# Performance work log

Hardware: AMD Instinct MI355X
Metric: run time of the kernel (lower is better)

The kernel has to match this reference:

```python
import jax, jax.numpy as jnp
import numpy as np

NUM_POINTS = 7
SCALES = (0.25, 0.125, 0.0625, 0.03125)
LENS_AREA = (8, 25)
OUTPUT_SIZES = ((8, 32), (8, 64))
CANON_SCALE = 224.0  # LevelMapper defaults (ctor's 160 is not forwarded)
CANON_LVL = 4.0
K_MIN, K_MAX = 2.0, 5.0
EPS = 1e-6


def _boundary_interp(pts, wp):
    # pts: [N, n, 2] polyline; sample wp points uniformly in arc parameter
    n = pts.shape[1]
    u = (jnp.arange(wp, dtype=pts.dtype) + 0.5) / wp * (n - 1)
    i0 = jnp.clip(jnp.floor(u).astype(jnp.int32), 0, n - 2)
    f = (u - i0.astype(pts.dtype))[None, :, None]
    return pts[:, i0] * (1 - f) + pts[:, i0 + 1] * f  # [N, wp, 2]


def _make_grid(polys_norm, hp, wp):
    # polys_norm: [N, 2n, 2] normalized to [0,1]; first n = top l->r, last n = bottom l->r
    n = polys_norm.shape[1] // 2
    top = _boundary_interp(polys_norm[:, :n], wp)
    bot = _boundary_interp(polys_norm[:, n:], wp)
    v = ((jnp.arange(hp, dtype=polys_norm.dtype) + 0.5) / hp)[None, :, None, None]
    return top[:, None] * (1 - v) + bot[:, None] * v  # [N, hp, wp, 2] (x,y)


def _bilinear(feat, img_ids, grid):
    # feat [B,C,H,W]; grid normalized [0,1] image coords -> pixel coords of this level
    B, C, H, W = feat.shape
    x = grid[..., 0] * W - 0.5
    y = grid[..., 1] * H - 0.5
    x0 = jnp.floor(x)
    y0 = jnp.floor(y)
    wx = (x - x0)[..., None]
    wy = (y - y0)[..., None]
    x0i = x0.astype(jnp.int32)
    y0i = y0.astype(jnp.int32)
    ids = img_ids[:, None, None]

    def g(xi, yi):
        xc = jnp.clip(xi, 0, W - 1)
        yc = jnp.clip(yi, 0, H - 1)
        val = feat[ids, :, yc, xc]  # [N, hp, wp, C]
        m = ((xi >= 0) & (xi < W) & (yi >= 0) & (yi < H))[..., None]
        return val * m.astype(feat.dtype)

    out = (g(x0i, y0i) * (1 - wx) * (1 - wy)
           + g(x0i + 1, y0i) * wx * (1 - wy)
           + g(x0i, y0i + 1) * (1 - wx) * wy
           + g(x0i + 1, y0i + 1) * wx * wy)
    return jnp.transpose(out, (0, 3, 1, 2))  # [N, C, hp, wp]


def _forward(feats, polys, img_ids, lens):
    n = NUM_POINTS
    idx = list(range(n)) + list(range(n, 2 * n))[::-1]  # top l->r, bottom flipped l->r
    H0, W0 = feats[0].shape[-2:]
    wh = jnp.array([W0 / SCALES[0], H0 / SCALES[0]], dtype=feats[0].dtype)
    polys_norm = polys[:, idx] / wh
    # FPN level routing from bbox area of the polygon (boxlist.area heuristic)
    s = jnp.sqrt((polys[..., 0].max(1) - polys[..., 0].min(1))
                 * (polys[..., 1].max(1) - polys[..., 1].min(1)))
    lvl = jnp.clip(jnp.floor(CANON_LVL + jnp.log2(s / CANON_SCALE + EPS)),
                   K_MIN, K_MAX).astype(jnp.int32) - int(K_MIN)
    # text-length bucket -> pooler id (first bucket whose len_max >= len)
    thr = jnp.array(LENS_AREA[:-1], dtype=lens.dtype)
    pooler_id = jnp.sum(lens[:, None] > thr[None, :], axis=1).astype(jnp.int32)

    outs = []
    N, C = polys.shape[0], feats[0].shape[1]
    for pid, (hp, wp) in enumerate(OUTPUT_SIZES):
        grid = _make_grid(polys_norm, hp, wp)
        acc = jnp.zeros((N, C, hp, wp), feats[0].dtype)
        for l, f in enumerate(feats):
            sel = ((lvl == l) & (pooler_id == pid))[:, None, None, None]
            acc = jnp.where(sel, _bilinear(f, img_ids, grid), acc)
        outs.append(acc)
    return tuple(outs)


def setup_inputs() -> dict:
    B, C, H0, W0 = 2, 256, 200, 336
    N, n = 256, NUM_POINTS
    key = jax.random.key(0)
    k0, k1, k2, k3 = jax.random.split(key, 4)
    feat0 = jax.random.normal(k0, (B, C, H0, W0), jnp.float32)
    feat1 = jax.random.normal(k1, (B, C, H0 // 2, W0 // 2), jnp.float32)
    feat2 = jax.random.normal(k2, (B, C, H0 // 4, W0 // 4), jnp.float32)
    feat3 = jax.random.normal(k3, (B, C, H0 // 8, W0 // 8), jnp.float32)
    rng = np.random.default_rng(0)
    img_w, img_h = W0 / SCALES[0], H0 / SCALES[0]
    cx = rng.uniform(0.25, 0.75, N) * img_w
    cy = rng.uniform(0.2, 0.8, N) * img_h
    w = rng.uniform(40.0, 600.0, N)
    h = rng.uniform(16.0, 80.0, N)
    t = np.linspace(0.0, 1.0, n)
    top_x = cx[:, None] + (t[None, :] - 0.5) * w[:, None]
    top_y = cy[:, None] - h[:, None] / 2 + rng.uniform(-2, 2, (N, n))
    bot_y = cy[:, None] + h[:, None] / 2 + rng.uniform(-2, 2, (N, n))
    # stored polygon order: top l->r then bottom r->l (matches self.idx reorder)
    top = np.stack([top_x, top_y], -1)
    bot = np.stack([top_x[:, ::-1], bot_y[:, ::-1]], -1)
    polys = jnp.asarray(np.concatenate([top, bot], 1), jnp.float32)  # [N, 14, 2]
    img_ids = jnp.asarray(rng.integers(0, B, N), jnp.int32)
    lens = jnp.asarray(rng.integers(1, 25, N), jnp.int32)
    return {"feat0": feat0, "feat1": feat1, "feat2": feat2, "feat3": feat3,
            "polys": polys, "img_ids": img_ids, "lens": lens}


def reference(feat0, feat1, feat2, feat3, polys, img_ids, lens):
    return _forward((feat0, feat1, feat2, feat3), polys, img_ids, lens)
```

## Files before the change

### kernel.cpp

```cpp
#include <hip/hip_runtime.h>


#define NBOX 256
#define NCH  256
#define HP   8
#define CCHUNK 32
#define OUT0_ELEMS ((size_t)NBOX * NCH * HP * 32)

typedef float f32x4 __attribute__((ext_vector_type(4)));

__device__ __forceinline__ void make_geo(
    const float* __restrict__ pts, int pos, int lwp, int W, int H,
    int& o00, int& o10, int& o01, int& o11,
    float& w00, float& w10, float& w01, float& w11)
{
    const int wp = 1 << lwp;
    const int i  = pos >> lwp;
    const int j  = pos & (wp - 1);

    float u  = ((j + 0.5f) / (float)wp) * 6.0f;
    int   i0 = (int)floorf(u);
    i0 = min(max(i0, 0), 5);
    float f = u - (float)i0;

    float txa = pts[2 * i0]     / 1344.0f, tya = pts[2 * i0 + 1] / 800.0f;
    float txb = pts[2 * i0 + 2] / 1344.0f, tyb = pts[2 * i0 + 3] / 800.0f;
    int ka = 13 - i0, kb = 12 - i0;
    float bxa = pts[2 * ka] / 1344.0f, bya = pts[2 * ka + 1] / 800.0f;
    float bxb = pts[2 * kb] / 1344.0f, byb = pts[2 * kb + 1] / 800.0f;

    float topx = txa * (1.0f - f) + txb * f;
    float topy = tya * (1.0f - f) + tyb * f;
    float botx = bxa * (1.0f - f) + bxb * f;
    float boty = bya * (1.0f - f) + byb * f;

    float v  = (i + 0.5f) / 8.0f;
    float gx = topx * (1.0f - v) + botx * v;
    float gy = topy * (1.0f - v) + boty * v;

    float x = gx * (float)W - 0.5f;
    float y = gy * (float)H - 0.5f;
    float x0f = floorf(x), y0f = floorf(y);
    float fx = x - x0f,   fy = y - y0f;
    int x0 = (int)x0f, y0 = (int)y0f;
    int x1 = x0 + 1,   y1 = y0 + 1;

    int x0c = min(max(x0, 0), W - 1), x1c = min(max(x1, 0), W - 1);
    int y0c = min(max(y0, 0), H - 1), y1c = min(max(y1, 0), H - 1);
    float m00 = (x0 >= 0 && x0 < W && y0 >= 0 && y0 < H) ? 1.0f : 0.0f;
    float m10 = (x1 >= 0 && x1 < W && y0 >= 0 && y0 < H) ? 1.0f : 0.0f;
    float m01 = (x0 >= 0 && x0 < W && y1 >= 0 && y1 < H) ? 1.0f : 0.0f;
    float m11 = (x1 >= 0 && x1 < W && y1 >= 0 && y1 < H) ? 1.0f : 0.0f;

    o00 = y0c * W + x0c;  o10 = y0c * W + x1c;
    o01 = y1c * W + x0c;  o11 = y1c * W + x1c;
    w00 = (1.0f - fx) * (1.0f - fy) * m00;
    w10 = fx * (1.0f - fy) * m10;
    w01 = (1.0f - fx) * fy * m01;
    w11 = fx * fy * m11;
}

__global__ __launch_bounds__(256) void poly_pool_kernel(
    const float* __restrict__ f0, const float* __restrict__ f1,
    const float* __restrict__ f2, const float* __restrict__ f3,
    const float* __restrict__ polys, const int* __restrict__ img_ids,
    const int* __restrict__ lens, float* __restrict__ out)
{
    const int b    = blockIdx.y;
    const int pidk = blockIdx.z;
    const int lwp  = 5 + pidk;
    const int npos = HP << lwp;
    const int c0   = blockIdx.x * CCHUNK;
    const int tid  = threadIdx.x;

    float* outb = out + (pidk ? OUT0_ELEMS : (size_t)0) + (size_t)b * NCH * npos;

    const int pooler = (lens[b] > 8) ? 1 : 0;
    if (pooler != pidk) {
        f32x4 z = (f32x4)(0.0f);
        f32x4* p = reinterpret_cast<f32x4*>(outb + (size_t)c0 * npos);
        const int total4 = (CCHUNK * npos) >> 2;
        for (int k = tid; k < total4; k += 256)
            __builtin_nontemporal_store(z, p + k);
        return;
    }

    __shared__ float pts[28];
    if (tid < 28) pts[tid] = polys[b * 28 + tid];
    __syncthreads();

    float minx = pts[0], maxx = pts[0], miny = pts[1], maxy = pts[1];
#pragma unroll
    for (int k = 1; k < 14; ++k) {
        float x = pts[2 * k], y = pts[2 * k + 1];
        minx = fminf(minx, x); maxx = fmaxf(maxx, x);
        miny = fminf(miny, y); maxy = fmaxf(maxy, y);
    }
    float s = sqrtf((maxx - minx) * (maxy - miny));
    int lvl = (int)floorf(4.0f + log2f(s / 224.0f + 1e-6f));
    lvl = min(max(lvl, 2), 5) - 2;

    const float* feat; int H, W;
    switch (lvl) {
        case 0:  feat = f0; H = 200; W = 336; break;
        case 1:  feat = f1; H = 100; W = 168; break;
        case 2:  feat = f2; H = 50;  W = 84;  break;
        default: feat = f3; H = 25;  W = 42;  break;
    }
    const int img = img_ids[b];
    const int HW  = H * W;
    const float* featimg = feat + (size_t)img * NCH * HW;
    const float* fbase   = featimg + (size_t)c0 * HW;

    int   o00, o10, o01, o11;
    float w00, w10, w01, w11;
    make_geo(pts, tid, lwp, W, H, o00, o10, o01, o11, w00, w10, w01, w11);

    float* op = outb + (size_t)c0 * npos + tid;

    if (!pidk) {
        for (int c = 0; c < CCHUNK; c += 8) {
            float t00[8], t10[8], t01[8], t11[8];
#pragma unroll
            for (int k = 0; k < 8; ++k) {
                const float* fc = fbase + (size_t)(c + k) * HW;
                t00[k] = fc[o00]; t10[k] = fc[o10];
                t01[k] = fc[o01]; t11[k] = fc[o11];
            }
#pragma unroll
            for (int k = 0; k < 8; ++k) {
                float r = w00 * t00[k] + w10 * t10[k] + w01 * t01[k] + w11 * t11[k];
                __builtin_nontemporal_store(r, op + (size_t)(c + k) * 256);
            }
        }
    } else {
        int   q00, q10, q01, q11;
        float v00, v10, v01, v11;
        make_geo(pts, tid + 256, lwp, W, H, q00, q10, q01, q11, v00, v10, v01, v11);

        for (int c = 0; c < CCHUNK; c += 4) {
            float t00[4], t10[4], t01[4], t11[4];
            float s00[4], s10[4], s01[4], s11[4];
#pragma unroll
            for (int k = 0; k < 4; ++k) {
                const float* fc = fbase + (size_t)(c + k) * HW;
                t00[k] = fc[o00]; t10[k] = fc[o10];
                t01[k] = fc[o01]; t11[k] = fc[o11];
                s00[k] = fc[q00]; s10[k] = fc[q10];
                s01[k] = fc[q01]; s11[k] = fc[q11];
            }
#pragma unroll
            for (int k = 0; k < 4; ++k) {
                float r0 = w00 * t00[k] + w10 * t10[k] + w01 * t01[k] + w11 * t11[k];
                float r1 = v00 * s00[k] + v10 * s10[k] + v01 * s01[k] + v11 * s11[k];
                __builtin_nontemporal_store(r0, op + (size_t)(c + k) * 512);
                __builtin_nontemporal_store(r1, op + (size_t)(c + k) * 512 + 256);
            }
        }
    }
}

extern "C" void kernel_launch(void* const* d_in, const int* in_sizes, int n_in,
                              void* d_out, int out_size, void* d_ws, size_t ws_size,
                              hipStream_t stream) {
    const float* f0    = (const float*)d_in[0];
    const float* f1    = (const float*)d_in[1];
    const float* f2    = (const float*)d_in[2];
    const float* f3    = (const float*)d_in[3];
    const float* polys = (const float*)d_in[4];
    const int*   ids   = (const int*)d_in[5];
    const int*   lens  = (const int*)d_in[6];
    float* out = (float*)d_out;

    dim3 grid(NCH / CCHUNK, NBOX, 2);
    poly_pool_kernel<<<grid, 256, 0, stream>>>(f0, f1, f2, f3, polys, ids, lens, out);
}
```

Before: 355.0 us.

## Stage polygon bounding-box feature patch in LDS before bilinear sampling

Computes the polygon's bounding box at the chosen FPN level and cooperatively loads that patch for 4 channels at a time into shared memory using coalesced row loads. The bilinear taps then read from LDS instead of doing scattered global gathers. Large patches fall back to a direct gather path. This adds 40KB of LDS per block, which lowers occupancy, plus two barriers per round and loads of patch pixels that may never be sampled.

```diff
diff --git a/kernel.cpp b/kernel.cpp
--- a/kernel.cpp
+++ b/kernel.cpp
@@ -5,13 +5,15 @@
 #define NCH  256
 #define HP   8
 #define CCHUNK 32
+#define NSTG 4
+#define PMAX 2560
 #define OUT0_ELEMS ((size_t)NBOX * NCH * HP * 32)
 
 typedef float f32x4 __attribute__((ext_vector_type(4)));
 
 __device__ __forceinline__ void make_geo(
     const float* __restrict__ pts, int pos, int lwp, int W, int H,
-    int& o00, int& o10, int& o01, int& o11,
+    int& x0c, int& x1c, int& y0c, int& y1c,
     float& w00, float& w10, float& w01, float& w11)
 {
     const int wp = 1 << lwp;
@@ -45,15 +47,13 @@
     int x0 = (int)x0f, y0 = (int)y0f;
     int x1 = x0 + 1,   y1 = y0 + 1;
 
-    int x0c = min(max(x0, 0), W - 1), x1c = min(max(x1, 0), W - 1);
-    int y0c = min(max(y0, 0), H - 1), y1c = min(max(y1, 0), H - 1);
+    x0c = min(max(x0, 0), W - 1); x1c = min(max(x1, 0), W - 1);
+    y0c = min(max(y0, 0), H - 1); y1c = min(max(y1, 0), H - 1);
     float m00 = (x0 >= 0 && x0 < W && y0 >= 0 && y0 < H) ? 1.0f : 0.0f;
     float m10 = (x1 >= 0 && x1 < W && y0 >= 0 && y0 < H) ? 1.0f : 0.0f;
     float m01 = (x0 >= 0 && x0 < W && y1 >= 0 && y1 < H) ? 1.0f : 0.0f;
     float m11 = (x1 >= 0 && x1 < W && y1 >= 0 && y1 < H) ? 1.0f : 0.0f;
 
-    o00 = y0c * W + x0c;  o10 = y0c * W + x1c;
-    o01 = y1c * W + x0c;  o11 = y1c * W + x1c;
     w00 = (1.0f - fx) * (1.0f - fy) * m00;
     w10 = fx * (1.0f - fy) * m10;
     w01 = (1.0f - fx) * fy * m01;
@@ -86,6 +86,7 @@
     }
 
     __shared__ float pts[28];
+    __shared__ float patch[NSTG][PMAX];
     if (tid < 28) pts[tid] = polys[b * 28 + tid];
     __syncthreads();
 
@@ -110,51 +111,92 @@
     const int img = img_ids[b];
     const int HW  = H * W;
     const float* featimg = feat + (size_t)img * NCH * HW;
-    const float* fbase   = featimg + (size_t)c0 * HW;
-
-    int   o00, o10, o01, o11;
+
+    float sxn = (float)W / 1344.0f, syn = (float)H / 800.0f;
+    int px0 = min(max((int)floorf(minx * sxn - 0.5f), 0), W - 1);
+    int px1 = min(max((int)floorf(maxx * sxn - 0.5f) + 1, 0), W - 1);
+    int py0 = min(max((int)floorf(miny * syn - 0.5f), 0), H - 1);
+    int py1 = min(max((int)floorf(maxy * syn - 0.5f) + 1, 0), H - 1);
+    const int PW = px1 - px0 + 1;
+    const int PH = py1 - py0 + 1;
+    const int lg = (PW <= 64) ? 6 : ((PW <= 128) ? 7 : 8);
+    const int PWP = 1 << lg;
+    const int npatch = PH << lg;
+    const bool staged = (PW <= 256) && (npatch <= PMAX);
+
+    int   x0c, x1c, y0c, y1c;
     float w00, w10, w01, w11;
-    make_geo(pts, tid, lwp, W, H, o00, o10, o01, o11, w00, w10, w01, w11);
+    make_geo(pts, tid, lwp, W, H, x0c, x1c, y0c, y1c, w00, w10, w01, w11);
+    int   x0d = 0, x1d = 0, y0d = 0, y1d = 0;
+    float v00 = 0, v10 = 0, v01 = 0, v11 = 0;
+    if (pidk)
+        make_geo(pts, tid + 256, lwp, W, H, x0d, x1d, y0d, y1d, v00, v10, v01, v11);
 
     float* op = outb + (size_t)c0 * npos + tid;
 
-    if (!pidk) {
-        for (int c = 0; c < CCHUNK; c += 8) {
-            float t00[8], t10[8], t01[8], t11[8];
+    if (staged) {
+        const int o00 = ((y0c - py0) << lg) + (x0c - px0);
+        const int o10 = ((y0c - py0) << lg) + (x1c - px0);
+        const int o01 = ((y1c - py0) << lg) + (x0c - px0);
+        const int o11 = ((y1c - py0) << lg) + (x1c - px0);
+        int q00 = 0, q10 = 0, q01 = 0, q11 = 0;
+        if (pidk) {
+            q00 = ((y0d - py0) << lg) + (x0d - px0);
+            q10 = ((y0d - py0) << lg) + (x1d - px0);
+            q01 = ((y1d - py0) << lg) + (x0d - px0);
+            q11 = ((y1d - py0) << lg) + (x1d - px0);
+        }
+
+        for (int rnd = 0; rnd < CCHUNK / NSTG; ++rnd) {
+            const float* sb = featimg + (size_t)(c0 + rnd * NSTG) * HW
+                              + (size_t)py0 * W + px0;
+            for (int e = tid; e < npatch; e += 512) {
+                int eb = min(e + 256, npatch - 1);
+                int ra = e  >> lg, ca = min(e  & (PWP - 1), PW - 1);
+                int rb = eb >> lg, cb = min(eb & (PWP - 1), PW - 1);
+                const float* sA = sb + ra * W + ca;
+                const float* sB = sb + rb * W + cb;
+                float a0 = sA[0], a1 = sA[HW], a2 = sA[2 * HW], a3 = sA[3 * HW];
+                float b0 = sB[0], b1 = sB[HW], b2 = sB[2 * HW], b3 = sB[3 * HW];
+                patch[0][e]  = a0; patch[1][e]  = a1;
+                patch[2][e]  = a2; patch[3][e]  = a3;
+                patch[0][eb] = b0; patch[1][eb] = b1;
+                patch[2][eb] = b2; patch[3][eb] = b3;
+            }
+            __syncthreads();
+
 #pragma unroll
-            for (int k = 0; k < 8; ++k) {
-                const float* fc = fbase + (size_t)(c + k) * HW;
-                t00[k] = fc[o00]; t10[k] = fc[o10];
-                t01[k] = fc[o01]; t11[k] = fc[o11];
-            }
+            for (int k = 0; k < NSTG; ++k) {
+                float r0 = w00 * patch[k][o00] + w10 * patch[k][o10]
+                         + w01 * patch[k][o01] + w11 * patch[k][o11];
+                __builtin_nontemporal_store(r0, op + (size_t)(rnd * NSTG + k) * npos);
+            }
+            if (pidk) {
 #pragma unroll
-            for (int k = 0; k < 8; ++k) {
-                float r = w00 * t00[k] + w10 * t10[k] + w01 * t01[k] + w11 * t11[k];
-                __builtin_nontemporal_store(r, op + (size_t)(c + k) * 256);
-            }
+                for (int k = 0; k < NSTG; ++k) {
+                    float r1 = v00 * patch[k][q00] + v10 * patch[k][q10]
+                             + v01 * patch[k][q01] + v11 * patch[k][q11];
+                    __builtin_nontemporal_store(r1, op + (size_t)(rnd * NSTG + k) * npos + 256);
+                }
+            }
+            __syncthreads();
         }
     } else {
-        int   q00, q10, q01, q11;
-        float v00, v10, v01, v11;
-        make_geo(pts, tid + 256, lwp, W, H, q00, q10, q01, q11, v00, v10, v01, v11);
-
-        for (int c = 0; c < CCHUNK; c += 4) {
-            float t00[4], t10[4], t01[4], t11[4];
-            float s00[4], s10[4], s01[4], s11[4];
-#pragma unroll
-            for (int k = 0; k < 4; ++k) {
-                const float* fc = fbase + (size_t)(c + k) * HW;
-                t00[k] = fc[o00]; t10[k] = fc[o10];
-                t01[k] = fc[o01]; t11[k] = fc[o11];
-                s00[k] = fc[q00]; s10[k] = fc[q10];
-                s01[k] = fc[q01]; s11[k] = fc[q11];
-            }
-#pragma unroll
-            for (int k = 0; k < 4; ++k) {
-                float r0 = w00 * t00[k] + w10 * t10[k] + w01 * t01[k] + w11 * t11[k];
-                float r1 = v00 * s00[k] + v10 * s10[k] + v01 * s01[k] + v11 * s11[k];
-                __builtin_nontemporal_store(r0, op + (size_t)(c + k) * 512);
-                __builtin_nontemporal_store(r1, op + (size_t)(c + k) * 512 + 256);
+        const int g00 = y0c * W + x0c, g10 = y0c * W + x1c;
+        const int g01 = y1c * W + x0c, g11 = y1c * W + x1c;
+        int h00 = 0, h10 = 0, h01 = 0, h11 = 0;
+        if (pidk) {
+            h00 = y0d * W + x0d; h10 = y0d * W + x1d;
+            h01 = y1d * W + x0d; h11 = y1d * W + x1d;
+        }
+        const float* fb = featimg + (size_t)c0 * HW;
+        for (int c = 0; c < CCHUNK; ++c) {
+            const float* fc = fb + (size_t)c * HW;
+            float r0 = w00 * fc[g00] + w10 * fc[g10] + w01 * fc[g01] + w11 * fc[g11];
+            __builtin_nontemporal_store(r0, op + (size_t)c * npos);
+            if (pidk) {
+                float r1 = v00 * fc[h00] + v10 * fc[h10] + v01 * fc[h01] + v11 * fc[h11];
+                __builtin_nontemporal_store(r1, op + (size_t)c * npos + 256);
             }
         }
     }
```

After: 344.0 us. -3.1%, faster.

## Stage polygon bounding-box feature patch in LDS and write float4 outputs

Applied to the files above, without the earlier changes.

Each block now copies the polygon's bounding-box patch of the feature map into shared memory, four channels at a time, and gathers the bilinear taps from shared memory instead of issuing scattered global loads. If the patch is too large, it falls back to direct global gathers. Each thread now computes four adjacent output positions and writes them as one vectorized float4 store, and the nontemporal stores are replaced by regular stores. The change adds two barriers per staging round, 20KB of LDS per block that may lower occupancy, and serial row-by-row staging using only PW threads.

```diff
diff --git a/kernel.cpp b/kernel.cpp
--- a/kernel.cpp
+++ b/kernel.cpp
@@ -5,12 +5,15 @@
 #define NCH  256
 #define HP   8
 #define CCHUNK 32
+#define NSTG 4
+#define PMAX 1280
 #define OUT0_ELEMS ((size_t)NBOX * NCH * HP * 32)
 
 typedef float f32x4 __attribute__((ext_vector_type(4)));
 
 __device__ __forceinline__ void make_geo(
     const float* __restrict__ pts, int pos, int lwp, int W, int H,
+    int pxo, int pyo, int PWe,
     int& o00, int& o10, int& o01, int& o11,
     float& w00, float& w10, float& w01, float& w11)
 {
@@ -52,8 +55,10 @@
     float m01 = (x0 >= 0 && x0 < W && y1 >= 0 && y1 < H) ? 1.0f : 0.0f;
     float m11 = (x1 >= 0 && x1 < W && y1 >= 0 && y1 < H) ? 1.0f : 0.0f;
 
-    o00 = y0c * W + x0c;  o10 = y0c * W + x1c;
-    o01 = y1c * W + x0c;  o11 = y1c * W + x1c;
+    o00 = (y0c - pyo) * PWe + (x0c - pxo);
+    o10 = (y0c - pyo) * PWe + (x1c - pxo);
+    o01 = (y1c - pyo) * PWe + (x0c - pxo);
+    o11 = (y1c - pyo) * PWe + (x1c - pxo);
     w00 = (1.0f - fx) * (1.0f - fy) * m00;
     w10 = fx * (1.0f - fy) * m10;
     w01 = (1.0f - fx) * fy * m01;
@@ -80,12 +85,12 @@
         f32x4 z = (f32x4)(0.0f);
         f32x4* p = reinterpret_cast<f32x4*>(outb + (size_t)c0 * npos);
         const int total4 = (CCHUNK * npos) >> 2;
-        for (int k = tid; k < total4; k += 256)
-            __builtin_nontemporal_store(z, p + k);
+        for (int k = tid; k < total4; k += 256) p[k] = z;
         return;
     }
 
     __shared__ float pts[28];
+    __shared__ float patch[NSTG][PMAX];
     if (tid < 28) pts[tid] = polys[b * 28 + tid];
     __syncthreads();
 
@@ -110,51 +115,82 @@
     const int img = img_ids[b];
     const int HW  = H * W;
     const float* featimg = feat + (size_t)img * NCH * HW;
-    const float* fbase   = featimg + (size_t)c0 * HW;
-
-    int   o00, o10, o01, o11;
-    float w00, w10, w01, w11;
-    make_geo(pts, tid, lwp, W, H, o00, o10, o01, o11, w00, w10, w01, w11);
-
-    float* op = outb + (size_t)c0 * npos + tid;
-
-    if (!pidk) {
-        for (int c = 0; c < CCHUNK; c += 8) {
-            float t00[8], t10[8], t01[8], t11[8];
-#pragma unroll
-            for (int k = 0; k < 8; ++k) {
-                const float* fc = fbase + (size_t)(c + k) * HW;
-                t00[k] = fc[o00]; t10[k] = fc[o10];
-                t01[k] = fc[o01]; t11[k] = fc[o11];
+
+    float sxn = (float)W / 1344.0f, syn = (float)H / 800.0f;
+    int px0 = min(max((int)floorf(minx * sxn - 0.5f), 0), W - 1);
+    int px1 = min(max((int)floorf(maxx * sxn - 0.5f) + 1, 0), W - 1);
+    int py0 = min(max((int)floorf(miny * syn - 0.5f), 0), H - 1);
+    int py1 = min(max((int)floorf(maxy * syn - 0.5f) + 1, 0), H - 1);
+    const int PW = px1 - px0 + 1;
+    const int PH = py1 - py0 + 1;
+    const int npatch = PH * PW;
+    const bool staged = (PW <= 256) && (npatch <= PMAX);
+
+    const int pxo = staged ? px0 : 0;
+    const int pyo = staged ? py0 : 0;
+    const int PWe = staged ? PW  : W;
+
+    const int pg   = tid & ((npos >> 2) - 1);
+    const int csub = tid >> (lwp + 1);
+    const int npass = pidk ? 2 : 1;
+
+    int   off[4][4];
+    float wt [4][4];
+#pragma unroll
+    for (int k = 0; k < 4; ++k)
+        make_geo(pts, 4 * pg + k, lwp, W, H, pxo, pyo, PWe,
+                 off[k][0], off[k][1], off[k][2], off[k][3],
+                 wt[k][0],  wt[k][1],  wt[k][2],  wt[k][3]);
+
+    if (staged) {
+        for (int rnd = 0; rnd < CCHUNK / NSTG; ++rnd) {
+            const float* sb = featimg + (size_t)(c0 + rnd * NSTG) * HW
+                              + (size_t)py0 * W + px0;
+            for (int r = 0; r < PH; r += 2) {
+                if (tid < PW) {
+                    const float* sA = sb + r * W + tid;
+                    float a0 = sA[0], a1 = sA[HW], a2 = sA[2 * HW], a3 = sA[3 * HW];
+                    const bool r1 = (r + 1 < PH);
+                    const float* sB = sA + W;
+                    float b0 = 0, b1 = 0, b2 = 0, b3 = 0;
+                    if (r1) { b0 = sB[0]; b1 = sB[HW]; b2 = sB[2 * HW]; b3 = sB[3 * HW]; }
+                    int d = r * PW + tid;
+                    patch[0][d] = a0; patch[1][d] = a1;
+                    patch[2][d] = a2; patch[3][d] = a3;
+                    if (r1) {
+                        int d2 = d + PW;
+                        patch[0][d2] = b0; patch[1][d2] = b1;
+                        patch[2][d2] = b2; patch[3][d2] = b3;
+                    }
+                }
             }
-#pragma unroll
-            for (int k = 0; k < 8; ++k) {
-                float r = w00 * t00[k] + w10 * t10[k] + w01 * t01[k] + w11 * t11[k];
-                __builtin_nontemporal_store(r, op + (size_t)(c + k) * 256);
+            __syncthreads();
+
+            for (int cc = 0; cc < npass; ++cc) {
+                const int slot = (cc << 1) + csub;
+                const float* pk = patch[slot];
+                f32x4 res;
+#pragma unroll
+                for (int k = 0; k < 4; ++k)
+                    res[k] = wt[k][0] * pk[off[k][0]] + wt[k][1] * pk[off[k][1]]
+                           + wt[k][2] * pk[off[k][2]] + wt[k][3] * pk[off[k][3]];
+                const int ch = c0 + (rnd << 2) + slot;
+                *reinterpret_cast<f32x4*>(outb + (size_t)ch * npos + (pg << 2)) = res;
             }
+            __syncthreads();
         }
     } else {
-        int   q00, q10, q01, q11;
-        float v00, v10, v01, v11;
-        make_geo(pts, tid + 256, lwp, W, H, q00, q10, q01, q11, v00, v10, v01, v11);
-
-        for (int c = 0; c < CCHUNK; c += 4) {
-            float t00[4], t10[4], t01[4], t11[4];
-            float s00[4], s10[4], s01[4], s11[4];
-#pragma unroll
-            for (int k = 0; k < 4; ++k) {
-                const float* fc = fbase + (size_t)(c + k) * HW;
-                t00[k] = fc[o00]; t10[k] = fc[o10];
-                t01[k] = fc[o01]; t11[k] = fc[o11];
-                s00[k] = fc[q00]; s10[k] = fc[q10];
-                s01[k] = fc[q01]; s11[k] = fc[q11];
-            }
-#pragma unroll
-            for (int k = 0; k < 4; ++k) {
-                float r0 = w00 * t00[k] + w10 * t10[k] + w01 * t01[k] + w11 * t11[k];
-                float r1 = v00 * s00[k] + v10 * s10[k] + v01 * s01[k] + v11 * s11[k];
-                __builtin_nontemporal_store(r0, op + (size_t)(c + k) * 512);
-                __builtin_nontemporal_store(r1, op + (size_t)(c + k) * 512 + 256);
+        for (int rnd = 0; rnd < CCHUNK / NSTG; ++rnd) {
+            for (int cc = 0; cc < npass; ++cc) {
+                const int slot = (cc << 1) + csub;
+                const int ch = c0 + (rnd << 2) + slot;
+                const float* fc = featimg + (size_t)ch * HW;
+                f32x4 res;
+#pragma unroll
+                for (int k = 0; k < 4; ++k)
+                    res[k] = wt[k][0] * fc[off[k][0]] + wt[k][1] * fc[off[k][1]]
+                           + wt[k][2] * fc[off[k][2]] + wt[k][3] * fc[off[k][3]];
+                *reinterpret_cast<f32x4*>(outb + (size_t)ch * npos + (pg << 2)) = res;
             }
         }
     }
```

Measured after the change: 397.0 us. 11.8% more time.

## Merge pooler blocks, vectorize output stores with 4 positions per thread

Applied to the files above, without the earlier changes.

Drops the z-dimension of the grid. Each block now zero-fills the unused pooler's output slice and computes the active pooler, which removes the half of blocks that only wrote zeros. Work is remapped so each thread computes 4 consecutive positions for one channel and writes them with a single 16-byte nontemporal store. The channel chunk shrinks to 16, launch bounds request 4 blocks per CU, and the geometry divides become multiplies by reciprocals. The cost is 16 gather loads per thread per round and more registers for the precomputed offsets and weights.

```diff
diff --git a/kernel.cpp b/kernel.cpp
--- a/kernel.cpp
+++ b/kernel.cpp
@@ -3,16 +3,14 @@
 
 #define NBOX 256
 #define NCH  256
-#define HP   8
-#define CCHUNK 32
-#define OUT0_ELEMS ((size_t)NBOX * NCH * HP * 32)
+#define CCHUNK 16
+#define OUT0_ELEMS ((size_t)NBOX * NCH * 8 * 32)
 
 typedef float f32x4 __attribute__((ext_vector_type(4)));
 
 __device__ __forceinline__ void make_geo(
     const float* __restrict__ pts, int pos, int lwp, int W, int H,
-    int& o00, int& o10, int& o01, int& o11,
-    float& w00, float& w10, float& w01, float& w11)
+    int* __restrict__ off, float* __restrict__ wt)
 {
     const int wp = 1 << lwp;
     const int i  = pos >> lwp;
@@ -23,11 +21,12 @@
     i0 = min(max(i0, 0), 5);
     float f = u - (float)i0;
 
-    float txa = pts[2 * i0]     / 1344.0f, tya = pts[2 * i0 + 1] / 800.0f;
-    float txb = pts[2 * i0 + 2] / 1344.0f, tyb = pts[2 * i0 + 3] / 800.0f;
+    const float inx = 1.0f / 1344.0f, iny = 1.0f / 800.0f;
+    float txa = pts[2 * i0]     * inx, tya = pts[2 * i0 + 1] * iny;
+    float txb = pts[2 * i0 + 2] * inx, tyb = pts[2 * i0 + 3] * iny;
     int ka = 13 - i0, kb = 12 - i0;
-    float bxa = pts[2 * ka] / 1344.0f, bya = pts[2 * ka + 1] / 800.0f;
-    float bxb = pts[2 * kb] / 1344.0f, byb = pts[2 * kb + 1] / 800.0f;
+    float bxa = pts[2 * ka] * inx, bya = pts[2 * ka + 1] * iny;
+    float bxb = pts[2 * kb] * inx, byb = pts[2 * kb + 1] * iny;
 
     float topx = txa * (1.0f - f) + txb * f;
     float topy = tya * (1.0f - f) + tyb * f;
@@ -52,42 +51,79 @@
     float m01 = (x0 >= 0 && x0 < W && y1 >= 0 && y1 < H) ? 1.0f : 0.0f;
     float m11 = (x1 >= 0 && x1 < W && y1 >= 0 && y1 < H) ? 1.0f : 0.0f;
 
-    o00 = y0c * W + x0c;  o10 = y0c * W + x1c;
-    o01 = y1c * W + x0c;  o11 = y1c * W + x1c;
-    w00 = (1.0f - fx) * (1.0f - fy) * m00;
-    w10 = fx * (1.0f - fy) * m10;
-    w01 = (1.0f - fx) * fy * m01;
-    w11 = fx * fy * m11;
+    off[0] = y0c * W + x0c;  off[1] = y0c * W + x1c;
+    off[2] = y1c * W + x0c;  off[3] = y1c * W + x1c;
+    wt[0] = (1.0f - fx) * (1.0f - fy) * m00;
+    wt[1] = fx * (1.0f - fy) * m10;
+    wt[2] = (1.0f - fx) * fy * m01;
+    wt[3] = fx * fy * m11;
 }
 
-__global__ __launch_bounds__(256) void poly_pool_kernel(
+template<int LWP>
+__device__ __forceinline__ void pool_real(
+    const float* __restrict__ featimg, int HW, int W, int H,
+    const float* __restrict__ pts, float* __restrict__ outR,
+    int c0, int tid)
+{
+    constexpr int NPOS   = 8 << LWP;
+    constexpr int GROUPS = NPOS / 4;
+    constexpr int SLOTS  = 256 / GROUPS;
+    constexpr int ROUNDS = CCHUNK / SLOTS;
+    const int pg   = tid & (GROUPS - 1);
+    const int csub = tid / GROUPS;
+
+    int   off[4][4];
+    float wt [4][4];
+#pragma unroll
+    for (int k = 0; k < 4; ++k)
+        make_geo(pts, 4 * pg + k, LWP, W, H, off[k], wt[k]);
+
+#pragma unroll 2
+    for (int r = 0; r < ROUNDS; ++r) {
+        const int ch = c0 + r * SLOTS + csub;
+        const float* fc = featimg + (size_t)ch * HW;
+        float t[4][4];
+#pragma unroll
+        for (int k = 0; k < 4; ++k)
+#pragma unroll
+            for (int j = 0; j < 4; ++j)
+                t[k][j] = fc[off[k][j]];
+        f32x4 res;
+#pragma unroll
+        for (int k = 0; k < 4; ++k)
+            res[k] = wt[k][0] * t[k][0] + wt[k][1] * t[k][1]
+                   + wt[k][2] * t[k][2] + wt[k][3] * t[k][3];
+        __builtin_nontemporal_store(res,
+            reinterpret_cast<f32x4*>(outR + (size_t)ch * NPOS + 4 * pg));
+    }
+}
+
+__global__ __launch_bounds__(256, 4) void poly_pool_kernel(
     const float* __restrict__ f0, const float* __restrict__ f1,
     const float* __restrict__ f2, const float* __restrict__ f3,
     const float* __restrict__ polys, const int* __restrict__ img_ids,
     const int* __restrict__ lens, float* __restrict__ out)
 {
-    const int b    = blockIdx.y;
-    const int pidk = blockIdx.z;
-    const int lwp  = 5 + pidk;
-    const int npos = HP << lwp;
-    const int c0   = blockIdx.x * CCHUNK;
-    const int tid  = threadIdx.x;
-
-    float* outb = out + (pidk ? OUT0_ELEMS : (size_t)0) + (size_t)b * NCH * npos;
-
-    const int pooler = (lens[b] > 8) ? 1 : 0;
-    if (pooler != pidk) {
-        f32x4 z = (f32x4)(0.0f);
-        f32x4* p = reinterpret_cast<f32x4*>(outb + (size_t)c0 * npos);
-        const int total4 = (CCHUNK * npos) >> 2;
-        for (int k = tid; k < total4; k += 256)
-            __builtin_nontemporal_store(z, p + k);
-        return;
-    }
+    const int b   = blockIdx.y;
+    const int c0  = blockIdx.x * CCHUNK;
+    const int tid = threadIdx.x;
 
     __shared__ float pts[28];
     if (tid < 28) pts[tid] = polys[b * 28 + tid];
     __syncthreads();
+
+    const int pid = (lens[b] > 8) ? 1 : 0;
+
+    {
+        const int nposZ = pid ? 256 : 512;
+        float* outZ = out + (pid ? (size_t)0 : OUT0_ELEMS)
+                    + (size_t)b * NCH * nposZ + (size_t)c0 * nposZ;
+        f32x4 z = (f32x4)(0.0f);
+        f32x4* p = reinterpret_cast<f32x4*>(outZ);
+        const int total4 = (CCHUNK * nposZ) >> 2;
+        for (int k = tid; k < total4; k += 256)
+            __builtin_nontemporal_store(z, p + k);
+    }
 
     float minx = pts[0], maxx = pts[0], miny = pts[1], maxy = pts[1];
 #pragma unroll
@@ -107,56 +143,15 @@
         case 2:  feat = f2; H = 50;  W = 84;  break;
         default: feat = f3; H = 25;  W = 42;  break;
     }
-    const int img = img_ids[b];
-    const int HW  = H * W;
-    const float* featimg = feat + (size_t)img * NCH * HW;
-    const float* fbase   = featimg + (size_t)c0 * HW;
+    const int HW = H * W;
+    const float* featimg = feat + (size_t)img_ids[b] * NCH * HW;
 
-    int   o00, o10, o01, o11;
-    float w00, w10, w01, w11;
-    make_geo(pts, tid, lwp, W, H, o00, o10, o01, o11, w00, w10, w01, w11);
-
-    float* op = outb + (size_t)c0 * npos + tid;
-
-    if (!pidk) {
-        for (int c = 0; c < CCHUNK; c += 8) {
-            float t00[8], t10[8], t01[8], t11[8];
-#pragma unroll
-            for (int k = 0; k < 8; ++k) {
-                const float* fc = fbase + (size_t)(c + k) * HW;
-                t00[k] = fc[o00]; t10[k] = fc[o10];
-                t01[k] = fc[o01]; t11[k] = fc[o11];
-            }
-#pragma unroll
-            for (int k = 0; k < 8; ++k) {
-                float r = w00 * t00[k] + w10 * t10[k] + w01 * t01[k] + w11 * t11[k];
-                __builtin_nontemporal_store(r, op + (size_t)(c + k) * 256);
-            }
-        }
+    if (pid == 0) {
+        float* outR = out + (size_t)b * NCH * 256;
+        pool_real<5>(featimg, HW, W, H, pts, outR, c0, tid);
     } else {
-        int   q00, q10, q01, q11;
-        float v00, v10, v01, v11;
-        make_geo(pts, tid + 256, lwp, W, H, q00, q10, q01, q11, v00, v10, v01, v11);
-
-        for (int c = 0; c < CCHUNK; c += 4) {
-            float t00[4], t10[4], t01[4], t11[4];
-            float s00[4], s10[4], s01[4], s11[4];
-#pragma unroll
-            for (int k = 0; k < 4; ++k) {
-                const float* fc = fbase + (size_t)(c + k) * HW;
-                t00[k] = fc[o00]; t10[k] = fc[o10];
-                t01[k] = fc[o01]; t11[k] = fc[o11];
-                s00[k] = fc[q00]; s10[k] = fc[q10];
-                s01[k] = fc[q01]; s11[k] = fc[q11];
-            }
-#pragma unroll
-            for (int k = 0; k < 4; ++k) {
-                float r0 = w00 * t00[k] + w10 * t10[k] + w01 * t01[k] + w11 * t11[k];
-                float r1 = v00 * s00[k] + v10 * s10[k] + v01 * s01[k] + v11 * s11[k];
-                __builtin_nontemporal_store(r0, op + (size_t)(c + k) * 512);
-                __builtin_nontemporal_store(r1, op + (size_t)(c + k) * 512 + 256);
-            }
-        }
+        float* outR = out + OUT0_ELEMS + (size_t)b * NCH * 512;
+        pool_real<6>(featimg, HW, W, H, pts, outR, c0, tid);
     }
 }
 
@@ -172,6 +167,6 @@
     const int*   lens  = (const int*)d_in[6];
     float* out = (float*)d_out;
 
-    dim3 grid(NCH / CCHUNK, NBOX, 2);
+    dim3 grid(NCH / CCHUNK, NBOX);
     poly_pool_kernel<<<grid, 256, 0, stream>>>(f0, f1, f2, f3, polys, ids, lens, out);
 }
```

Result: slower. 370.6 us (+4.4%).
